# Performance work log

Hardware: AMD Instinct MI355X
Metric: run time of the kernel (lower is better)

## Reference

```python
import jax, jax.numpy as jnp
import numpy as np

B, L, D = 4, 2048, 512


def setup_inputs() -> dict:
    key = jax.random.key(0)
    ks = jax.random.split(key, 12)
    f32 = jnp.float32
    mk = lambda k, s: jax.random.normal(k, s, dtype=f32)
    # xavier-uniform-ish init scale for the linear weights
    w_qkv_lim = np.sqrt(6.0 / (6 * D + 6 * D)).astype(np.float32)
    w_out_lim = np.sqrt(6.0 / (2 * D + 2 * D)).astype(np.float32)
    return {
        "q_real": mk(ks[0], (B, L, D)),
        "q_imag": mk(ks[1], (B, L, D)),
        "k_real": mk(ks[2], (B, L, D)),
        "k_imag": mk(ks[3], (B, L, D)),
        "v_real": mk(ks[4], (B, L, D)),
        "v_imag": mk(ks[5], (B, L, D)),
        "pad_mask": jax.random.randint(ks[6], (B, L), 0, 2).astype(jnp.bool_),
        "W_qkv": jax.random.uniform(ks[7], (6 * D, 6 * D), f32, -w_qkv_lim, w_qkv_lim),
        "b_qkv": jnp.zeros((6 * D,), f32),
        "W_out": jax.random.uniform(ks[8], (2 * D, 2 * D), f32, -w_out_lim, w_out_lim),
        "b_out": jnp.zeros((2 * D,), f32),
    }


def reference(q_real, q_imag, k_real, k_imag, v_real, v_imag, pad_mask,
              W_qkv, b_qkv, W_out, b_out):
    b, l, d = q_real.shape
    # fused QKV projection over concatenated real/imag streams: [B, L, 6D]
    x = jnp.concatenate([q_real, q_imag, k_real, k_imag, v_real, v_imag], axis=-1)
    qkv = x @ W_qkv.T + b_qkv                      # torch Linear: x @ W^T + b
    qkv = qkv.reshape(b, l, 6, d)
    q_r, k_r = qkv[:, :, 0], qkv[:, :, 2]
    v_r, v_i = qkv[:, :, 4], qkv[:, :, 5]
    scale = jnp.asarray(d, jnp.float32) ** -0.5
    scores = jnp.einsum('bqd,bkd->bqk', q_r, k_r) * scale   # [B, L, L]
    scores = jnp.where(pad_mask[:, None, :], -jnp.inf, scores)
    attn = jax.nn.softmax(scores, axis=-1)         # dropout omitted (eval mode)
    out_real = jnp.einsum('bqk,bkd->bqd', attn, v_r)
    out_imag = jnp.einsum('bqk,bkd->bqd', attn, v_i)
    out = jnp.concatenate([out_real, out_imag], axis=-1) @ W_out.T + b_out
    return out[..., :d], out[..., d:]
```

## Files before the change

kernel.cpp:

```cpp
#include <hip/hip_runtime.h>
#include <cstdint>
#include <cstddef>

typedef unsigned short ushort;
typedef __attribute__((ext_vector_type(8))) short short8;
typedef __attribute__((ext_vector_type(16))) float f32x16;

__device__ __forceinline__ float bf2f(ushort u) {
  union { unsigned u; float f; } c; c.u = ((unsigned)u) << 16; return c.f;
}
__device__ __forceinline__ ushort f2bf(float f) {
  union { float f; unsigned u; } c; c.f = f;
  unsigned u = c.u;
  return (ushort)((u + 0x7fffu + ((u >> 16) & 1u)) >> 16);
}

#define G2L(g, l) __builtin_amdgcn_global_load_lds( \
    (const __attribute__((address_space(1))) void*)(g), \
    (__attribute__((address_space(3))) void*)(l), 16, 0, 0)

#define BARRIER() do { asm volatile("" ::: "memory"); __builtin_amdgcn_s_barrier(); asm volatile("" ::: "memory"); } while (0)
#define LGKMC(N) do { asm volatile("s_waitcnt lgkmcnt(%0)" :: "n"(N) : "memory"); __builtin_amdgcn_sched_barrier(0); } while (0)

__device__ __forceinline__ unsigned ldsoff(const void* p) {
  return (unsigned)(unsigned long long)(__attribute__((address_space(3))) const void*)p;
}

struct MArgs {
  const ushort* A; int lda; long asz;
  const ushort* B; int ldb; long bsz;
  void* C; int ldc; long csz;
  int K;
  const float* bias;
  float* C2;
};

template<int MODE, int BN>
__launch_bounds__(512, 2)
__global__ void mfma_gemm(MArgs g) {
  constexpr int BM = 256;
  constexpr int WN = BN / 64;
  constexpr int WM = 8 / WN;
  constexpr int WMSZ = BM / WM;
  constexpr int MF = WMSZ / 32;
  constexpr int NBG = BN / 64;
  constexpr int LPS = 4 + NBG;
  constexpr int RD = MF + 2;

  __shared__ __attribute__((aligned(16))) ushort As[2][BM * 64];
  __shared__ __attribute__((aligned(16))) ushort Bs[2][BN * 64];

  const int tid = threadIdx.x;
  const int lane = tid & 63;
  const int wave = tid >> 6;
  const int z = blockIdx.z;

  int bx = blockIdx.x, by = blockIdx.y;
  {
    const int gx = gridDim.x;
    const int nwg = gx * gridDim.y;
    int wg = by * gx + bx;
    wg = (wg & 7) * (nwg >> 3) + (wg >> 3);
    bx = wg % gx; by = wg / gx;
  }
  const long m0 = (long)by * BM;
  const long n0 = (long)bx * BN;
  const ushort* Ab = g.A + (long)z * g.asz;
  const ushort* Bb = g.B + (long)z * g.bsz;

  const int srow = tid >> 3;
  const long skel = (long)((((tid & 7) - srow) & 7) * 8);
  const ushort* ga[4];
  const ushort* gb[NBG];
#pragma unroll
  for (int q = 0; q < 4; ++q) ga[q] = Ab + (m0 + q * 64 + srow) * (long)g.lda + skel;
#pragma unroll
  for (int q = 0; q < NBG; ++q) gb[q] = Bb + (n0 + q * 64 + srow) * (long)g.ldb + skel;

  const int l31 = lane & 31, hb = lane >> 5;
  const int wmi = wave / WN, wni = wave % WN;
  unsigned aoffB[MF]; int arot[MF];
#pragma unroll
  for (int mf = 0; mf < MF; ++mf) {
    const int r = wmi * WMSZ + mf * 32 + l31;
    aoffB[mf] = (unsigned)(r * 128);
    arot[mf] = (r + hb) & 7;
  }
  unsigned boffB[2]; int brot[2];
#pragma unroll
  for (int nf = 0; nf < 2; ++nf) {
    const int r = wni * 64 + nf * 32 + l31;
    boffB[nf] = (unsigned)(r * 128);
    brot[nf] = (r + hb) & 7;
  }

  f32x16 acc[MF][2];
#pragma unroll
  for (int mf = 0; mf < MF; ++mf)
#pragma unroll
    for (int nf = 0; nf < 2; ++nf)
#pragma unroll
      for (int r = 0; r < 16; ++r) acc[mf][nf][r] = 0.f;

  auto STAGEF = [&](int buf, int t) {
    const long ko = (long)t * 64;
#pragma unroll
    for (int q = 0; q < 4; ++q) G2L(ga[q] + ko, &As[buf][q * 4096 + tid * 8]);
#pragma unroll
    for (int q = 0; q < NBG; ++q) G2L(gb[q] + ko, &Bs[buf][q * 4096 + tid * 8]);
  };

  STAGEF(0, 0);
  STAGEF(1, 1);

  const int nt = g.K >> 6;
  for (int t = 0; t < nt; ++t) {
    const int cur = t & 1;
    if (t + 1 < nt) asm volatile("s_waitcnt vmcnt(%0)" :: "n"(LPS) : "memory");
    else            asm volatile("s_waitcnt vmcnt(0)" ::: "memory");
    BARRIER();

    const unsigned abase = ldsoff(&As[cur][0]);
    const unsigned bbase = ldsoff(&Bs[cur][0]);
    short8 av[2][MF], bv[2][2];

#define ISSUE_H(s, h) do { \
  _Pragma("unroll") for (int mf = 0; mf < MF; ++mf) { \
    unsigned o = abase + aoffB[mf] + (unsigned)((((2 * (h) + arot[mf]) & 7) << 4)); \
    asm volatile("ds_read_b128 %0, %1" : "=v"(av[s][mf]) : "v"(o)); \
  } \
  _Pragma("unroll") for (int nf = 0; nf < 2; ++nf) { \
    unsigned o = bbase + boffB[nf] + (unsigned)((((2 * (h) + brot[nf]) & 7) << 4)); \
    asm volatile("ds_read_b128 %0, %1" : "=v"(bv[s][nf]) : "v"(o)); \
  } \
} while (0)
#define MFMA_S(s) do { \
  __builtin_amdgcn_s_setprio(1); \
  _Pragma("unroll") for (int mf = 0; mf < MF; ++mf) \
  _Pragma("unroll") for (int nf = 0; nf < 2; ++nf) \
    acc[mf][nf] = __builtin_amdgcn_mfma_f32_32x32x16_bf16(av[s][mf], bv[s][nf], acc[mf][nf], 0, 0, 0); \
  __builtin_amdgcn_s_setprio(0); \
} while (0)

    ISSUE_H(0, 0);
    ISSUE_H(1, 1);
    LGKMC(RD);
    MFMA_S(0);
    ISSUE_H(0, 2);
    LGKMC(RD);
    MFMA_S(1);
    ISSUE_H(1, 3);
    LGKMC(RD);
    MFMA_S(0);
    LGKMC(0);
    BARRIER();
    if (t + 2 < nt) STAGEF(cur, t + 2);
    MFMA_S(1);
#undef ISSUE_H
#undef MFMA_S
  }

  const int cc = l31;
  const int rbase = 4 * hb;
  ushort* Cu = (ushort*)g.C + (long)z * g.csz;
  float* Cf = (float*)g.C;
#pragma unroll
  for (int mf = 0; mf < MF; ++mf) {
#pragma unroll
    for (int nf = 0; nf < 2; ++nf) {
      const long col = n0 + wni * 64 + nf * 32 + cc;
      float bsv = 0.f;
      if (MODE == 0 || MODE == 3) bsv = g.bias[col];
#pragma unroll
      for (int r = 0; r < 16; ++r) {
        const long row = m0 + wmi * WMSZ + mf * 32 + (r & 3) + 8 * (r >> 2) + rbase;
        float v = acc[mf][nf][r] + bsv;
        if (MODE == 3) {
          float* dst = (col < 512) ? (Cf + row * 512 + col) : (g.C2 + row * 512 + (col - 512));
          *dst = v;
        } else {
          Cu[row * (long)g.ldc + col] = f2bf(v);
        }
      }
    }
  }
}

__global__ void cvt_x6(const float* x0, const float* x1, const float* x2,
                       const float* x3, const float* x4, const float* x5, ushort* X) {
  const long m = blockIdx.y;
  const int c4 = (blockIdx.x * 256 + threadIdx.x) * 4;
  const int p = c4 >> 9, d = c4 & 511;
  const float* xp;
  switch (p) {
    case 0: xp = x0; break; case 1: xp = x1; break; case 2: xp = x2; break;
    case 3: xp = x3; break; case 4: xp = x4; break; default: xp = x5; break;
  }
  float4 v = *(const float4*)(xp + m * 512 + d);
  ushort4 o; o.x = f2bf(v.x); o.y = f2bf(v.y); o.z = f2bf(v.z); o.w = f2bf(v.w);
  *(ushort4*)(X + m * 3072 + c4) = o;
}

__device__ __forceinline__ int chunk_map(int c) { return (c == 0) ? 0 : (c == 1) ? 2 : (c == 2) ? 4 : 5; }

__global__ void cvt_w4(const float* W, ushort* Wq4) {
  const long r = blockIdx.y;
  const int c4 = (blockIdx.x * 256 + threadIdx.x) * 4;
  const long wr = (long)chunk_map((int)(r >> 9)) * 512 + (r & 511);
  float4 v = *(const float4*)(W + wr * 3072 + c4);
  ushort4 o; o.x = f2bf(v.x); o.y = f2bf(v.y); o.z = f2bf(v.z); o.w = f2bf(v.w);
  *(ushort4*)(Wq4 + r * 3072 + c4) = o;
}

__global__ void cvt_wout(const float* W, ushort* Wo) {
  const long r = blockIdx.y;
  const int c4 = threadIdx.x * 4;
  float4 v = *(const float4*)(W + r * 1024 + c4);
  ushort4 o; o.x = f2bf(v.x); o.y = f2bf(v.y); o.z = f2bf(v.z); o.w = f2bf(v.w);
  *(ushort4*)(Wo + r * 1024 + c4) = o;
}

__global__ void mk_bias4(const float* bqkv, float* b4) {
  const int n = blockIdx.x * 256 + threadIdx.x;
  b4[n] = bqkv[chunk_map(n >> 9) * 512 + (n & 511)];
}

__global__ void transpose_v(const ushort* QKV, ushort* Vt) {
  __shared__ ushort t[64][65];
  const int tid = threadIdx.x;
  const int k0 = blockIdx.x * 64, n0 = blockIdx.y * 64, b = blockIdx.z;
  const ushort* src = QKV + (long)b * 2048 * 2048 + 1024;
#pragma unroll
  for (int i = 0; i < 16; ++i) {
    int idx = i * 256 + tid; int r = idx >> 6, c = idx & 63;
    t[r][c] = src[(long)(k0 + r) * 2048 + (n0 + c)];
  }
  __syncthreads();
  ushort* dst = Vt + (long)b * 1024 * 2048;
#pragma unroll
  for (int i = 0; i < 16; ++i) {
    int idx = i * 256 + tid; int r = idx >> 6, c = idx & 63;
    dst[(long)(n0 + r) * 2048 + (k0 + c)] = t[c][r];
  }
}

__launch_bounds__(256)
__global__ void softmax_rows(ushort* S, const int* mask) {
  const int lane = threadIdx.x & 63;
  const int wave = threadIdx.x >> 6;
  const long row = (long)blockIdx.x * 4 + wave;
  const int* m = mask + (row >> 11) * 2048 + lane * 32;
  ushort* s = S + row * 2048 + lane * 32;
  const float scale = 0.04419417382415922f;

  short8 raw[4];
#pragma unroll
  for (int i = 0; i < 4; ++i) raw[i] = *(const short8*)(s + i * 8);
  int4 mi[8];
#pragma unroll
  for (int i = 0; i < 8; ++i) mi[i] = *(const int4*)(m + i * 4);

  float v[32];
  int mk[32];
#pragma unroll
  for (int i = 0; i < 8; ++i) {
    mk[i * 4 + 0] = mi[i].x; mk[i * 4 + 1] = mi[i].y;
    mk[i * 4 + 2] = mi[i].z; mk[i * 4 + 3] = mi[i].w;
  }
#pragma unroll
  for (int i = 0; i < 32; ++i) v[i] = bf2f((ushort)raw[i >> 3][i & 7]) * scale;

  float mx = -INFINITY;
#pragma unroll
  for (int i = 0; i < 32; ++i) if (!mk[i]) mx = fmaxf(mx, v[i]);
#pragma unroll
  for (int off = 32; off; off >>= 1) mx = fmaxf(mx, __shfl_xor(mx, off));

  float sum = 0.f;
#pragma unroll
  for (int i = 0; i < 32; ++i) {
    float e = mk[i] ? 0.f : __expf(v[i] - mx);
    v[i] = e;
    sum += e;
  }
#pragma unroll
  for (int off = 32; off; off >>= 1) sum += __shfl_xor(sum, off);

  float r = 1.f / sum;
  short8 out[4];
#pragma unroll
  for (int i = 0; i < 32; ++i) out[i >> 3][i & 7] = (short)f2bf(v[i] * r);
#pragma unroll
  for (int i = 0; i < 4; ++i) *(short8*)(s + i * 8) = out[i];
}

extern "C" void kernel_launch(void* const* d_in, const int* in_sizes, int n_in,
                              void* d_out, int out_size, void* d_ws, size_t ws_size,
                              hipStream_t stream) {
  const float* qr = (const float*)d_in[0];
  const float* qi = (const float*)d_in[1];
  const float* kr = (const float*)d_in[2];
  const float* ki = (const float*)d_in[3];
  const float* vr = (const float*)d_in[4];
  const float* vi = (const float*)d_in[5];
  const int* pm = (const int*)d_in[6];
  const float* Wqkv = (const float*)d_in[7];
  const float* bqkv = (const float*)d_in[8];
  const float* Wout = (const float*)d_in[9];
  const float* bout = (const float*)d_in[10];
  float* out = (float*)d_out;

  char* base = (char*)d_ws;
  ushort* QKV   = (ushort*)(base);
  ushort* Wq4   = (ushort*)(base + 33554432);
  ushort* Wo    = (ushort*)(base + 46137344);
  float*  b4    = (float*) (base + 48234496);
  char*   uni   = base + 48242688;
  ushort* Xbf   = (ushort*)(uni);
  ushort* Vt    = (ushort*)(uni);
  ushort* S     = (ushort*)(uni + 16777216);
  ushort* AO    = (ushort*)(uni + 50331648);

  cvt_x6<<<dim3(3, 8192), 256, 0, stream>>>(qr, qi, kr, ki, vr, vi, Xbf);
  cvt_w4<<<dim3(3, 2048), 256, 0, stream>>>(Wqkv, Wq4);
  cvt_wout<<<dim3(1, 1024), 256, 0, stream>>>(Wout, Wo);
  mk_bias4<<<8, 256, 0, stream>>>(bqkv, b4);

  {
    MArgs a{};
    a.A = Xbf; a.lda = 3072; a.asz = 0;
    a.B = Wq4; a.ldb = 3072; a.bsz = 0;
    a.C = QKV; a.ldc = 2048; a.csz = 0;
    a.K = 3072; a.bias = b4;
    mfma_gemm<0, 256><<<dim3(8, 32, 1), 512, 0, stream>>>(a);
  }

  transpose_v<<<dim3(32, 16, 4), 256, 0, stream>>>(QKV, Vt);

  {
    MArgs a{};
    a.A = QKV;        a.lda = 2048; a.asz = (long)2048 * 2048;
    a.B = QKV + 512;  a.ldb = 2048; a.bsz = (long)2048 * 2048;
    a.C = S;          a.ldc = 2048; a.csz = (long)2048 * 2048;
    a.K = 512;
    mfma_gemm<1, 256><<<dim3(8, 8, 4), 512, 0, stream>>>(a);
  }

  softmax_rows<<<2048, 256, 0, stream>>>(S, pm);

  {
    MArgs a{};
    a.A = S;  a.lda = 2048; a.asz = (long)2048 * 2048;
    a.B = Vt; a.ldb = 2048; a.bsz = (long)1024 * 2048;
    a.C = AO; a.ldc = 1024; a.csz = (long)2048 * 1024;
    a.K = 2048;
    mfma_gemm<2, 128><<<dim3(8, 8, 4), 512, 0, stream>>>(a);
  }

  {
    MArgs a{};
    a.A = AO; a.lda = 1024; a.asz = 0;
    a.B = Wo; a.ldb = 1024; a.bsz = 0;
    a.C = out; a.ldc = 512; a.csz = 0;
    a.C2 = out + (long)8192 * 512;
    a.K = 1024; a.bias = bout;
    mfma_gemm<3, 128><<<dim3(8, 32, 1), 512, 0, stream>>>(a);
  }
}
```

Baseline: 391.8 us.

## Prefetch next tile's first LDS fragments before final MFMA and vectorize V transpose

Restructures the GEMM main loop so the next tile's stage is waited on, barriered, and its first half of LDS fragments read before the last MFMA batch of the current tile. This hides LDS read latency across tile boundaries, at the cost of an extra barrier per iteration. The V transpose kernel now uses 16-byte global loads and stores with a padded shared tile, where it previously used scalar 2-byte accesses.

```diff
diff --git a/kernel.cpp b/kernel.cpp
--- a/kernel.cpp
+++ b/kernel.cpp
@@ -110,27 +110,17 @@
     for (int q = 0; q < NBG; ++q) G2L(gb[q] + ko, &Bs[buf][q * 4096 + tid * 8]);
   };
 
-  STAGEF(0, 0);
-  STAGEF(1, 1);
-
-  const int nt = g.K >> 6;
-  for (int t = 0; t < nt; ++t) {
-    const int cur = t & 1;
-    if (t + 1 < nt) asm volatile("s_waitcnt vmcnt(%0)" :: "n"(LPS) : "memory");
-    else            asm volatile("s_waitcnt vmcnt(0)" ::: "memory");
-    BARRIER();
-
-    const unsigned abase = ldsoff(&As[cur][0]);
-    const unsigned bbase = ldsoff(&Bs[cur][0]);
-    short8 av[2][MF], bv[2][2];
-
-#define ISSUE_H(s, h) do { \
+  const unsigned abB[2] = { ldsoff(&As[0][0]), ldsoff(&As[1][0]) };
+  const unsigned bbB[2] = { ldsoff(&Bs[0][0]), ldsoff(&Bs[1][0]) };
+  short8 av[2][MF], bv[2][2];
+
+#define ISSUE_H(s, h, ab, bb) do { \
   _Pragma("unroll") for (int mf = 0; mf < MF; ++mf) { \
-    unsigned o = abase + aoffB[mf] + (unsigned)((((2 * (h) + arot[mf]) & 7) << 4)); \
+    unsigned o = (ab) + aoffB[mf] + (unsigned)((((2 * (h) + arot[mf]) & 7) << 4)); \
     asm volatile("ds_read_b128 %0, %1" : "=v"(av[s][mf]) : "v"(o)); \
   } \
   _Pragma("unroll") for (int nf = 0; nf < 2; ++nf) { \
-    unsigned o = bbase + boffB[nf] + (unsigned)((((2 * (h) + brot[nf]) & 7) << 4)); \
+    unsigned o = (bb) + boffB[nf] + (unsigned)((((2 * (h) + brot[nf]) & 7) << 4)); \
     asm volatile("ds_read_b128 %0, %1" : "=v"(bv[s][nf]) : "v"(o)); \
   } \
 } while (0)
@@ -142,23 +132,43 @@
   __builtin_amdgcn_s_setprio(0); \
 } while (0)
 
-    ISSUE_H(0, 0);
-    ISSUE_H(1, 1);
+  STAGEF(0, 0);
+  STAGEF(1, 1);
+  asm volatile("s_waitcnt vmcnt(%0)" :: "n"(LPS) : "memory");
+  BARRIER();
+  ISSUE_H(0, 0, abB[0], bbB[0]);
+
+  const int nt = g.K >> 6;
+  for (int t = 0; t < nt; ++t) {
+    const int cur = t & 1;
+    const unsigned ab = abB[cur], bb = bbB[cur];
+
+    ISSUE_H(1, 1, ab, bb);
     LGKMC(RD);
     MFMA_S(0);
-    ISSUE_H(0, 2);
+    ISSUE_H(0, 2, ab, bb);
     LGKMC(RD);
     MFMA_S(1);
-    ISSUE_H(1, 3);
+    ISSUE_H(1, 3, ab, bb);
     LGKMC(RD);
     MFMA_S(0);
     LGKMC(0);
-    BARRIER();
-    if (t + 2 < nt) STAGEF(cur, t + 2);
+
+    if (t + 1 < nt) {
+      BARRIER();
+      if (t + 2 < nt) {
+        STAGEF(cur, t + 2);
+        asm volatile("s_waitcnt vmcnt(%0)" :: "n"(LPS) : "memory");
+      } else {
+        asm volatile("s_waitcnt vmcnt(0)" ::: "memory");
+      }
+      BARRIER();
+      ISSUE_H(0, 0, abB[cur ^ 1], bbB[cur ^ 1]);
+    }
     MFMA_S(1);
+  }
 #undef ISSUE_H
 #undef MFMA_S
-  }
 
   const int cc = l31;
   const int rbase = 4 * hb;
@@ -226,21 +236,28 @@
 }
 
 __global__ void transpose_v(const ushort* QKV, ushort* Vt) {
-  __shared__ ushort t[64][65];
+  __shared__ ushort t2[64][68];
   const int tid = threadIdx.x;
   const int k0 = blockIdx.x * 64, n0 = blockIdx.y * 64, b = blockIdx.z;
   const ushort* src = QKV + (long)b * 2048 * 2048 + 1024;
 #pragma unroll
-  for (int i = 0; i < 16; ++i) {
-    int idx = i * 256 + tid; int r = idx >> 6, c = idx & 63;
-    t[r][c] = src[(long)(k0 + r) * 2048 + (n0 + c)];
+  for (int i = 0; i < 2; ++i) {
+    const int slot = i * 256 + tid;
+    const int kr = slot >> 3, nc = slot & 7;
+    short8 v = *(const short8*)(src + (long)(k0 + kr) * 2048 + (n0 + nc * 8));
+#pragma unroll
+    for (int j = 0; j < 8; ++j) t2[nc * 8 + j][kr] = (ushort)v[j];
   }
   __syncthreads();
   ushort* dst = Vt + (long)b * 1024 * 2048;
 #pragma unroll
-  for (int i = 0; i < 16; ++i) {
-    int idx = i * 256 + tid; int r = idx >> 6, c = idx & 63;
-    dst[(long)(n0 + r) * 2048 + (k0 + c)] = t[c][r];
+  for (int i = 0; i < 2; ++i) {
+    const int slot = i * 256 + tid;
+    const int nr = slot >> 3, kc = slot & 7;
+    short8 v;
+#pragma unroll
+    for (int j = 0; j < 8; ++j) v[j] = (short)t2[nr][kc * 8 + j];
+    *(short8*)(dst + (long)(n0 + nr) * 2048 + (k0 + kc * 8)) = v;
   }
 }
 
```

Measured after the change: 387.9 us. Within noise of the previous version (-1.0%).
